# Optimization experiments

Measured on AMD Instinct MI355X. Metric: run time of the kernel, lower is better.

Reference implementation:

```python
import jax, jax.numpy as jnp
import numpy as np

N_NODES = 65536
N_EDGES = 1048576
D_IN = 1024
D_HID = 64
N_CLS = 32


def gcn_conv(x, W, b, src, dst, n_nodes):
    """PyG GCNConv: linear transform, then symmetric-normalized aggregation
    with implicit self-loops (fill value 1)."""
    xw = x @ W  # [N, d_out]
    e = src.shape[0]
    # degree over destination index, including the self-loop (+1)
    deg = jax.ops.segment_sum(jnp.ones((e,), xw.dtype), dst, num_segments=n_nodes) + 1.0
    dinv_sqrt = jax.lax.rsqrt(deg)  # deg >= 1, safe
    norm = dinv_sqrt[src] * dinv_sqrt[dst]  # [E]
    agg = jax.ops.segment_sum(xw[src] * norm[:, None], dst, num_segments=n_nodes)
    # self-loop contribution: norm = deg_i^{-1}
    agg = agg + xw * (1.0 / deg)[:, None]
    return agg + b


def setup_inputs() -> dict:
    key = jax.random.key(0)
    k_x, k_e, k_w1, k_b1, k_w2, k_b2 = jax.random.split(key, 6)
    x = jax.random.normal(k_x, (N_NODES, D_IN), dtype=jnp.float32)
    edge_index = jax.random.randint(k_e, (2, N_EDGES), 0, N_NODES, dtype=jnp.int64)
    s1 = 1.0 / np.sqrt(D_IN)
    s2 = 1.0 / np.sqrt(D_HID)
    W1 = jax.random.uniform(k_w1, (D_IN, D_HID), jnp.float32, -s1, s1)
    b1 = jax.random.uniform(k_b1, (D_HID,), jnp.float32, -s1, s1)
    W2 = jax.random.uniform(k_w2, (D_HID, N_CLS), jnp.float32, -s2, s2)
    b2 = jax.random.uniform(k_b2, (N_CLS,), jnp.float32, -s2, s2)
    return {"x": x, "edge_index": edge_index, "W1": W1, "b1": b1, "W2": W2, "b2": b2}


def reference(x, edge_index, W1, b1, W2, b2):
    src, dst = edge_index[0], edge_index[1]
    n = x.shape[0]
    h = gcn_conv(x, W1, b1, src, dst, n)
    h = jax.nn.relu(h)
    # dropout is identity in eval mode
    h = gcn_conv(h, W2, b2, src, dst, n)
    return jax.nn.log_softmax(h, axis=1)
```

## Files before the change

### kernel.cpp

```cpp
#include <hip/hip_runtime.h>
#include <hip/hip_bf16.h>

#define N_NODES 65536
#define D_IN 1024
#define D_HID 64
#define N_CLS 32
#define NBUK 256
#define NSB 256

typedef short short8 __attribute__((ext_vector_type(8)));
typedef float floatx4 __attribute__((ext_vector_type(4)));

__device__ __forceinline__ unsigned short f2bf(float f) {
  union { float f; unsigned u; } cv; cv.f = f;
  unsigned r = (cv.u + 0x7FFFu + ((cv.u >> 16) & 1u)) >> 16;
  return (unsigned short)r;
}
__device__ __forceinline__ float2 bf2f2(unsigned v) {
  union { unsigned u; float f; } a, b;
  a.u = v << 16;
  b.u = v & 0xFFFF0000u;
  return make_float2(a.f, b.f);
}

__global__ void k_hist_w1t(const int* __restrict__ dst, int* __restrict__ H,
                           const float* __restrict__ w1, unsigned short* __restrict__ w1t,
                           int e4) {
  int b = blockIdx.x, t = threadIdx.x;
  if (b >= NSB) {
    int i = (b - NSB) * 256 + t;
    int k = i / D_HID, n = i % D_HID;
    w1t[n * D_IN + k] = f2bf(w1[i]);
    return;
  }
  __shared__ int hist[NBUK];
  hist[t] = 0;
  __syncthreads();
  const int4* d4 = (const int4*)dst + b * 1024;
#pragma unroll
  for (int p = 0; p < 4; p++) {
    int i4 = b * 1024 + p * 256 + t;
    if (i4 < e4) {
      int4 d = d4[p * 256 + t];
      atomicAdd(&hist[d.x >> 8], 1);
      atomicAdd(&hist[d.y >> 8], 1);
      atomicAdd(&hist[d.z >> 8], 1);
      atomicAdd(&hist[d.w >> 8], 1);
    }
  }
  __syncthreads();
  H[b * NBUK + t] = hist[t];
}

__global__ void k_scan_bin(const int* __restrict__ H, int* __restrict__ Hs,
                           int* __restrict__ btot) {
  int bin = blockIdx.x, t = threadIdx.x;
  int v = H[t * NBUK + bin];
  __shared__ int s[256];
  s[t] = v;
  __syncthreads();
  for (int off = 1; off < 256; off <<= 1) {
    int x = (t >= off) ? s[t - off] : 0;
    __syncthreads();
    s[t] += x;
    __syncthreads();
  }
  Hs[bin * NSB + t] = s[t] - v;
  if (t == 255) btot[bin] = s[255];
}

__global__ void k_scan_tot(const int* __restrict__ btot, int* __restrict__ btoff,
                           int* __restrict__ rowptr, int e) {
  __shared__ int s[256];
  int t = threadIdx.x;
  int v = btot[t];
  s[t] = v;
  __syncthreads();
  for (int off = 1; off < 256; off <<= 1) {
    int x = (t >= off) ? s[t - off] : 0;
    __syncthreads();
    s[t] += x;
    __syncthreads();
  }
  btoff[t] = s[t] - v;
  if (t == 0) rowptr[N_NODES] = e;
}

__global__ __launch_bounds__(256) void k_scatter(
    const int* __restrict__ dst, const int* __restrict__ src,
    const int* __restrict__ Hs, const int* __restrict__ btoff,
    unsigned* __restrict__ pk, int e4) {
  __shared__ int cnt[NBUK], sc[NBUK], cur[NBUK], base2[NBUK];
  __shared__ unsigned stage[4096];
  int b = blockIdx.x, t = threadIdx.x;
  cnt[t] = 0;
  __syncthreads();
  const int4* d4 = (const int4*)dst + b * 1024;
  const int4* s4 = (const int4*)src + b * 1024;
  int4 dv[4], sv[4]; bool ok[4];
#pragma unroll
  for (int p = 0; p < 4; p++) {
    int i4 = b * 1024 + p * 256 + t;
    ok[p] = i4 < e4;
    if (ok[p]) {
      dv[p] = d4[p * 256 + t];
      sv[p] = s4[p * 256 + t];
      atomicAdd(&cnt[dv[p].x >> 8], 1);
      atomicAdd(&cnt[dv[p].y >> 8], 1);
      atomicAdd(&cnt[dv[p].z >> 8], 1);
      atomicAdd(&cnt[dv[p].w >> 8], 1);
    }
  }
  __syncthreads();
  int c = cnt[t];
  sc[t] = c;
  __syncthreads();
  for (int off = 1; off < 256; off <<= 1) {
    int xv = (t >= off) ? sc[t - off] : 0;
    __syncthreads();
    sc[t] += xv;
    __syncthreads();
  }
  int excl = sc[t] - c;
  cur[t] = excl;
  base2[t] = btoff[t] + Hs[t * NSB + b] - excl;
  __syncthreads();
  int tot = sc[255];
#pragma unroll
  for (int p = 0; p < 4; p++) {
    if (ok[p]) {
      int d[4] = {dv[p].x, dv[p].y, dv[p].z, dv[p].w};
      int s[4] = {sv[p].x, sv[p].y, sv[p].z, sv[p].w};
#pragma unroll
      for (int j = 0; j < 4; j++) {
        int pos = atomicAdd(&cur[d[j] >> 8], 1);
        stage[pos] = ((unsigned)d[j] << 16) | (unsigned)s[j];
      }
    }
  }
  __syncthreads();
  for (int i = t; i < tot; i += 256) {
    unsigned u = stage[i];
    pk[base2[u >> 24] + i] = u;
  }
}

__global__ void k_bucket_csr(const unsigned* __restrict__ pk, const int* __restrict__ btoff,
                             const int* __restrict__ btot, int* __restrict__ rowptr,
                             int* __restrict__ csr_src, float* __restrict__ dinv) {
  __shared__ int cnt[NBUK], sc[NBUK], cur[NBUK];
  int bin = blockIdx.x, t = threadIdx.x;
  cnt[t] = 0;
  __syncthreads();
  int beg = btoff[bin], len = btot[bin];
  for (int i = t; i < len; i += 256)
    atomicAdd(&cnt[(pk[beg + i] >> 16) & 255], 1);
  __syncthreads();
  int c = cnt[t];
  sc[t] = c;
  __syncthreads();
  for (int off = 1; off < 256; off <<= 1) {
    int x = (t >= off) ? sc[t - off] : 0;
    __syncthreads();
    sc[t] += x;
    __syncthreads();
  }
  int excl = sc[t] - c;
  int node = bin * 256 + t;
  rowptr[node] = beg + excl;
  dinv[node] = rsqrtf((float)(c + 1));
  cur[t] = excl;
  __syncthreads();
  for (int i = t; i < len; i += 256) {
    unsigned u = pk[beg + i];
    int p = atomicAdd(&cur[(u >> 16) & 255], 1);
    csr_src[beg + p] = (int)(u & 0xFFFFu);
  }
}

#define GCHUNK(PA, KC) do {                                                    \
    float4 c0 = PA[0], c1 = PA[1], c2 = PA[2], c3 = PA[3];                     \
    if ((KC) + 128 < D_IN) {                                                   \
      PA[0] = *(const float4*)(xrow + (KC) + 128);                             \
      PA[1] = *(const float4*)(xrow + (KC) + 132);                             \
      PA[2] = *(const float4*)(xrow + (KC) + 160);                             \
      PA[3] = *(const float4*)(xrow + (KC) + 164);                             \
    }                                                                          \
    int kb = ((KC) + 64 < D_IN) ? (KC) + 64 : (KC);                            \
    float av0[8] = {c0.x, c0.y, c0.z, c0.w, c1.x, c1.y, c1.z, c1.w};           \
    float av1[8] = {c2.x, c2.y, c2.z, c2.w, c3.x, c3.y, c3.z, c3.w};           \
    short8 af0, af1;                                                           \
    unsigned* u0 = (unsigned*)&af0;                                            \
    unsigned* u1 = (unsigned*)&af1;                                            \
    _Pragma("unroll") for (int j = 0; j < 4; j++) {                            \
      asm("v_cvt_pk_bf16_f32 %0, %1, %2"                                       \
          : "=v"(u0[j]) : "v"(av0[2 * j]), "v"(av0[2 * j + 1]));               \
      asm("v_cvt_pk_bf16_f32 %0, %1, %2"                                       \
          : "=v"(u1[j]) : "v"(av1[2 * j]), "v"(av1[2 * j + 1]));               \
    }                                                                          \
    _Pragma("unroll") for (int nt = 0; nt < 4; nt++)                           \
      acc[nt] = __builtin_amdgcn_mfma_f32_16x16x32_bf16(af0, bf0[nt], acc[nt], 0, 0, 0); \
    _Pragma("unroll") for (int nt = 0; nt < 4; nt++)                           \
      bf0[nt] = *(const short8*)(bbase + (size_t)(nt * 16 + l16) * D_IN + kb); \
    _Pragma("unroll") for (int nt = 0; nt < 4; nt++)                           \
      acc[nt] = __builtin_amdgcn_mfma_f32_16x16x32_bf16(af1, bf1[nt], acc[nt], 0, 0, 0); \
    _Pragma("unroll") for (int nt = 0; nt < 4; nt++)                           \
      bf1[nt] = *(const short8*)(bbase + (size_t)(nt * 16 + l16) * D_IN + kb + 32); \
  } while (0)

__global__ __launch_bounds__(256) void k_gemm1(
    const float* __restrict__ x, const unsigned short* __restrict__ w1t,
    unsigned short* __restrict__ xw1s) {
  int rb = blockIdx.x;
  if (rb >= 1024) rb -= 1024;
  int wave = threadIdx.x >> 6;
  int lane = threadIdx.x & 63;
  int quad = lane >> 4;
  int l16 = lane & 15;
  int rowbase = rb * 64 + wave * 16;
  const float* xrow = x + (size_t)(rowbase + l16) * D_IN + quad * 8;
  const unsigned short* bbase = w1t + quad * 8;
  floatx4 acc[4];
#pragma unroll
  for (int nt = 0; nt < 4; nt++) acc[nt] = (floatx4){0.f, 0.f, 0.f, 0.f};
  float4 pa0[4], pa1[4];
  pa0[0] = *(const float4*)(xrow + 0);
  pa0[1] = *(const float4*)(xrow + 4);
  pa0[2] = *(const float4*)(xrow + 32);
  pa0[3] = *(const float4*)(xrow + 36);
  pa1[0] = *(const float4*)(xrow + 64);
  pa1[1] = *(const float4*)(xrow + 68);
  pa1[2] = *(const float4*)(xrow + 96);
  pa1[3] = *(const float4*)(xrow + 100);
  short8 bf0[4], bf1[4];
#pragma unroll
  for (int nt = 0; nt < 4; nt++) {
    const unsigned short* bp = bbase + (size_t)(nt * 16 + l16) * D_IN;
    bf0[nt] = *(const short8*)(bp);
    bf1[nt] = *(const short8*)(bp + 32);
  }
#pragma unroll
  for (int k0 = 0; k0 < D_IN; k0 += 128) {
    GCHUNK(pa0, k0);
    GCHUNK(pa1, k0 + 64);
  }
#pragma unroll
  for (int r = 0; r < 4; r++) {
    int row = rowbase + quad * 4 + r;
#pragma unroll
    for (int nt = 0; nt < 4; nt++)
      xw1s[(size_t)row * D_HID + nt * 16 + l16] = f2bf(acc[nt][r]);
  }
}

__global__ __launch_bounds__(256) void k_agg1(const unsigned* __restrict__ xw1s2,
    const int* __restrict__ rowptr, const int* __restrict__ csr_src,
    const float* __restrict__ dinv, const float* __restrict__ b1,
    const float* __restrict__ w2, unsigned short* __restrict__ xw2s) {
  __shared__ float w2s[D_HID * N_CLS];
  for (int i = threadIdx.x; i < D_HID * N_CLS; i += 256) w2s[i] = w2[i];
  __syncthreads();
  int wave = threadIdx.x >> 6;
  int lane = threadIdx.x & 63;
  int h = lane >> 5, l = lane & 31;
  int node = blockIdx.x * 4 + wave;
  float dd = dinv[node];
  int beg = rowptr[node], end = rowptr[node + 1];
  float cx[8], cy[8];
#pragma unroll
  for (int j = 0; j < 8; j++) { cx[j] = 0.f; cy[j] = 0.f; }
  for (int e = beg + h; e < end; e += 16) {
    int idx[8]; bool val[8];
#pragma unroll
    for (int j = 0; j < 8; j++) {
      int ee = e + 2 * j;
      val[j] = ee < end;
      idx[j] = csr_src[val[j] ? ee : beg];
    }
    float dv[8];
#pragma unroll
    for (int j = 0; j < 8; j++) dv[j] = dinv[idx[j]];
#pragma unroll
    for (int j = 0; j < 8; j++) {
      float2 v = bf2f2(xw1s2[(size_t)idx[j] * 32 + l]);
      float w = val[j] ? dv[j] : 0.f;
      cx[j] += w * v.x;
      cy[j] += w * v.y;
    }
  }
  float sx = ((cx[0] + cx[1]) + (cx[2] + cx[3])) + ((cx[4] + cx[5]) + (cx[6] + cx[7]));
  float sy = ((cy[0] + cy[1]) + (cy[2] + cy[3])) + ((cy[4] + cy[5]) + (cy[6] + cy[7]));
  sx += __shfl_xor(sx, 32);
  sy += __shfl_xor(sy, 32);
  float2 self = bf2f2(xw1s2[(size_t)node * 32 + l]);
  float2 bb = ((const float2*)b1)[l];
  float vx = dd * (sx + dd * self.x) + bb.x;
  float vy = dd * (sy + dd * self.y) + bb.y;
  vx = vx > 0.f ? vx : 0.f;
  vy = vy > 0.f ? vy : 0.f;
  int c = lane & 31;
  float p = 0.f;
#pragma unroll
  for (int kk = 0; kk < 32; kk++) {
    int k = h * 32 + kk;
    float hv = (k & 1) ? __shfl(vy, k >> 1) : __shfl(vx, k >> 1);
    p += hv * w2s[k * N_CLS + c];
  }
  p += __shfl_xor(p, 32);
  if (lane < 32) xw2s[(size_t)node * N_CLS + c] = f2bf(p * dd);
}

__global__ __launch_bounds__(256) void k_agg2(const unsigned* __restrict__ xw2s2,
    const int* __restrict__ rowptr, const int* __restrict__ csr_src,
    const float* __restrict__ dinv, const float* __restrict__ b2,
    float* __restrict__ out) {
  int wave = threadIdx.x >> 6;
  int lane = threadIdx.x & 63;
  int q = lane >> 4, l = lane & 15;
  int node = blockIdx.x * 4 + wave;
  float dd = dinv[node];
  int beg = rowptr[node], end = rowptr[node + 1];
  float cx[4], cy[4];
#pragma unroll
  for (int j = 0; j < 4; j++) { cx[j] = 0.f; cy[j] = 0.f; }
  for (int e = beg + q; e < end; e += 16) {
    int idx[4]; bool val[4];
#pragma unroll
    for (int j = 0; j < 4; j++) {
      int ee = e + 4 * j;
      val[j] = ee < end;
      idx[j] = csr_src[val[j] ? ee : beg];
    }
#pragma unroll
    for (int j = 0; j < 4; j++) {
      float2 v = bf2f2(xw2s2[(size_t)idx[j] * 16 + l]);
      cx[j] += val[j] ? v.x : 0.f;
      cy[j] += val[j] ? v.y : 0.f;
    }
  }
  float sx = (cx[0] + cx[1]) + (cx[2] + cx[3]);
  float sy = (cy[0] + cy[1]) + (cy[2] + cy[3]);
  sx += __shfl_xor(sx, 32); sy += __shfl_xor(sy, 32);
  sx += __shfl_xor(sx, 16); sy += __shfl_xor(sy, 16);
  float2 self = bf2f2(xw2s2[(size_t)node * 16 + l]);
  float2 bb = ((const float2*)b2)[l];
  float lx = dd * (sx + self.x) + bb.x;
  float ly = dd * (sy + self.y) + bb.y;
  float m = fmaxf(lx, ly);
#pragma unroll
  for (int o = 8; o > 0; o >>= 1) m = fmaxf(m, __shfl_xor(m, o));
  float s2 = __expf(lx - m) + __expf(ly - m);
#pragma unroll
  for (int o = 8; o > 0; o >>= 1) s2 += __shfl_xor(s2, o);
  float lse = m + __logf(s2);
  if (lane < 16)
    ((float2*)out)[(size_t)node * 16 + l] = make_float2(lx - lse, ly - lse);
}

extern "C" void kernel_launch(void* const* d_in, const int* in_sizes, int n_in,
                              void* d_out, int out_size, void* d_ws, size_t ws_size,
                              hipStream_t stream) {
  (void)n_in; (void)out_size; (void)ws_size;
  const float* x  = (const float*)d_in[0];
  const int*   ei = (const int*)d_in[1];
  const float* w1 = (const float*)d_in[2];
  const float* b1 = (const float*)d_in[3];
  const float* w2 = (const float*)d_in[4];
  const float* b2 = (const float*)d_in[5];
  float* out = (float*)d_out;
  int e = in_sizes[1] / 2;
  const int* src = ei;
  const int* dst = ei + e;

  char* ws = (char*)d_ws;
  int* H              = (int*)(ws + 0x0000000);
  int* Hs             = (int*)(ws + 0x0040000);
  int* btot           = (int*)(ws + 0x0080000);
  int* btoff          = (int*)(ws + 0x0080400);
  int* rowptr         = (int*)(ws + 0x0081000);
  float* dinv         = (float*)(ws + 0x00D0000);
  unsigned* pk        = (unsigned*)(ws + 0x0200000);
  int* csr_src        = (int*)(ws + 0x0600000);
  unsigned short* w1t = (unsigned short*)(ws + 0x0A00000);
  unsigned short* xw1s= (unsigned short*)(ws + 0x0A20000);
  unsigned short* xw2s= (unsigned short*)(ws + 0x1220000);

  int e4 = e / 4;
  k_hist_w1t  <<<NSB + 256, 256, 0, stream>>>(dst, H, w1, w1t, e4);
  k_scan_bin  <<<NBUK, 256, 0, stream>>>(H, Hs, btot);
  k_scan_tot  <<<1, 256, 0, stream>>>(btot, btoff, rowptr, e);
  k_scatter   <<<NSB, 256, 0, stream>>>(dst, src, Hs, btoff, pk, e4);
  k_bucket_csr<<<NBUK, 256, 0, stream>>>(pk, btoff, btot, rowptr, csr_src, dinv);
  k_gemm1     <<<2048, 256, 0, stream>>>(x, w1t, xw1s);
  k_agg1      <<<N_NODES / 4, 256, 0, stream>>>((const unsigned*)xw1s, rowptr, csr_src,
                                                dinv, b1, w2, xw2s);
  k_agg2      <<<N_NODES / 4, 256, 0, stream>>>((const unsigned*)xw2s, rowptr, csr_src,
                                                dinv, b2, out);
}
```

Before: 600.3 us.

## Split GEMM1 K dimension across wave pairs with shared-memory reduction

Each k_gemm1 block now covers 32 rows instead of 64. Two waves compute the first half of K (0–511) and two compute the second half. The second-half partial accumulators go through shared memory and are summed by the first-half waves before the bf16 store. This also removes the old grid mapping, where blocks 1024–2047 recomputed the same row blocks as 0–1023, so x is now read only once. It gains per-wave parallelism and shorter dependent MFMA chains, at the cost of 8 KB of shared memory per block and a block-wide barrier.

```diff
diff --git a/kernel.cpp b/kernel.cpp
--- a/kernel.cpp
+++ b/kernel.cpp
@@ -180,13 +180,13 @@
 
 #define GCHUNK(PA, KC) do {                                                    \
     float4 c0 = PA[0], c1 = PA[1], c2 = PA[2], c3 = PA[3];                     \
-    if ((KC) + 128 < D_IN) {                                                   \
+    if ((KC) + 128 < 512) {                                                    \
       PA[0] = *(const float4*)(xrow + (KC) + 128);                             \
       PA[1] = *(const float4*)(xrow + (KC) + 132);                             \
       PA[2] = *(const float4*)(xrow + (KC) + 160);                             \
       PA[3] = *(const float4*)(xrow + (KC) + 164);                             \
     }                                                                          \
-    int kb = ((KC) + 64 < D_IN) ? (KC) + 64 : (KC);                            \
+    int kb = ((KC) + 64 < 512) ? (KC) + 64 : (KC);                             \
     float av0[8] = {c0.x, c0.y, c0.z, c0.w, c1.x, c1.y, c1.z, c1.w};           \
     float av1[8] = {c2.x, c2.y, c2.z, c2.w, c3.x, c3.y, c3.z, c3.w};           \
     short8 af0, af1;                                                           \
@@ -211,15 +211,17 @@
 __global__ __launch_bounds__(256) void k_gemm1(
     const float* __restrict__ x, const unsigned short* __restrict__ w1t,
     unsigned short* __restrict__ xw1s) {
-  int rb = blockIdx.x;
-  if (rb >= 1024) rb -= 1024;
+  __shared__ float red[2][16][64];
   int wave = threadIdx.x >> 6;
   int lane = threadIdx.x & 63;
   int quad = lane >> 4;
   int l16 = lane & 15;
-  int rowbase = rb * 64 + wave * 16;
-  const float* xrow = x + (size_t)(rowbase + l16) * D_IN + quad * 8;
-  const unsigned short* bbase = w1t + quad * 8;
+  int rowgrp = wave & 1;
+  int kh = wave >> 1;
+  int rowbase = blockIdx.x * 32 + rowgrp * 16;
+  int kbeg = kh * 512;
+  const float* xrow = x + (size_t)(rowbase + l16) * D_IN + kbeg + quad * 8;
+  const unsigned short* bbase = w1t + kbeg + quad * 8;
   floatx4 acc[4];
 #pragma unroll
   for (int nt = 0; nt < 4; nt++) acc[nt] = (floatx4){0.f, 0.f, 0.f, 0.f};
@@ -240,16 +242,28 @@
     bf1[nt] = *(const short8*)(bp + 32);
   }
 #pragma unroll
-  for (int k0 = 0; k0 < D_IN; k0 += 128) {
+  for (int k0 = 0; k0 < 512; k0 += 128) {
     GCHUNK(pa0, k0);
     GCHUNK(pa1, k0 + 64);
   }
-#pragma unroll
-  for (int r = 0; r < 4; r++) {
-    int row = rowbase + quad * 4 + r;
+  if (kh == 1) {
 #pragma unroll
     for (int nt = 0; nt < 4; nt++)
-      xw1s[(size_t)row * D_HID + nt * 16 + l16] = f2bf(acc[nt][r]);
+#pragma unroll
+      for (int r = 0; r < 4; r++)
+        red[rowgrp][quad * 4 + r][nt * 16 + l16] = acc[nt][r];
+  }
+  __syncthreads();
+  if (kh == 0) {
+#pragma unroll
+    for (int r = 0; r < 4; r++) {
+      int row = rowbase + quad * 4 + r;
+#pragma unroll
+      for (int nt = 0; nt < 4; nt++) {
+        float v = acc[nt][r] + red[rowgrp][quad * 4 + r][nt * 16 + l16];
+        xw1s[(size_t)row * D_HID + nt * 16 + l16] = f2bf(v);
+      }
+    }
   }
 }
 
@@ -391,7 +405,7 @@
   k_scan_tot  <<<1, 256, 0, stream>>>(btot, btoff, rowptr, e);
   k_scatter   <<<NSB, 256, 0, stream>>>(dst, src, Hs, btoff, pk, e4);
   k_bucket_csr<<<NBUK, 256, 0, stream>>>(pk, btoff, btot, rowptr, csr_src, dinv);
-  k_gemm1     <<<2048, 256, 0, stream>>>(x, w1t, xw1s);
+  k_gemm1     <<<N_NODES / 32, 256, 0, stream>>>(x, w1t, xw1s);
   k_agg1      <<<N_NODES / 4, 256, 0, stream>>>((const unsigned*)xw1s, rowptr, csr_src,
                                                 dinv, b1, w2, xw2s);
   k_agg2      <<<N_NODES / 4, 256, 0, stream>>>((const unsigned*)xw2s, rowptr, csr_src,
```

New measurement: 508.4 us. 15.3% less time.
